# Performance work log

Measured on AMD Instinct MI355X. Metric: run time of the kernel, lower is better.

## Reference

```python
import jax, jax.numpy as jnp
import numpy as np

N, H, W = 8, 64, 64
CIN = 512    # latent_size_prev == conv_insize
COUT = 512   # latent_size == conv_outsize
Z = 512      # latent vector dim


def setup_inputs() -> dict:
    key = jax.random.key(0)
    ks = jax.random.split(key, 6)
    data = jax.random.normal(ks[0], (N, H, W, CIN), dtype=jnp.float32)
    latent = jax.random.normal(ks[1], (N, Z), dtype=jnp.float32)
    dense_w = jax.random.normal(ks[2], (Z, CIN), dtype=jnp.float32)
    dense_b = jnp.ones((CIN,), dtype=jnp.float32)  # ones_initializer per StyleBlock2
    conv_w = jax.random.normal(ks[3], (3, 3, CIN, COUT), dtype=jnp.float32)
    bias = jnp.zeros((1, 1, 1, COUT), dtype=jnp.float32)
    noise_coef = jnp.zeros((1, 1, 1, COUT), dtype=jnp.float32)
    noise = jax.random.normal(ks[4], (N, H, W, COUT), dtype=jnp.float32)
    return {"data": data, "latent": latent, "dense_w": dense_w, "dense_b": dense_b,
            "conv_w": conv_w, "bias": bias, "noise_coef": noise_coef, "noise": noise}


def reference(data, latent, dense_w, dense_b, conv_w, bias, noise_coef, noise):
    # ScaledDense: style vector s = latent @ (W * sqrt(2/Z)) + b
    dense_coef = jnp.sqrt(2.0 / Z).astype(data.dtype)
    s = latent @ (dense_w * dense_coef) + dense_b           # [N, CIN]

    # modulate input by style
    x = data * s[:, None, None, :]                          # [N,H,W,CIN]

    conv_coef = jnp.sqrt(2.0 / (CIN * 9)).astype(data.dtype)
    w = conv_w * conv_coef                                  # [3,3,CIN,COUT]
    y = jax.lax.conv_general_dilated(
        x, w, window_strides=(1, 1), padding='SAME',
        dimension_numbers=('NHWC', 'HWIO', 'NHWC'))         # [N,H,W,COUT]

    # demodulation: sum_{k,k,cin} (w * s)^2 == (s^2) @ sum_{k,k} w^2
    w2 = jnp.sum(w * w, axis=(0, 1))                        # [CIN, COUT]
    d = jax.lax.rsqrt((s * s) @ w2 + 1e-8)                  # [N, COUT]
    y = y * d[:, None, None, :]

    y = y + bias + noise * noise_coef
    return jnp.where(y >= 0, y, 0.2 * y)  # leaky relu, alpha=0.2
```

## Files before the change

### kernel.cpp

```cpp
#include <hip/hip_runtime.h>
#include <stdint.h>

typedef unsigned short ushort_t;
typedef unsigned int uint_t;
typedef __bf16 bf16x8 __attribute__((ext_vector_type(8)));
typedef float f32x4 __attribute__((ext_vector_type(4)));

#define C2F 0.02083333333333333f

__device__ __forceinline__ float bf2f(unsigned short u) {
  union { unsigned int i; float f; } v; v.i = ((unsigned int)u) << 16; return v.f;
}
__device__ __forceinline__ unsigned short f2bf(float f) {
  union { float f; unsigned int i; } v; v.f = f;
  unsigned int r = v.i + 0x7FFFu + ((v.i >> 16) & 1u);
  return (unsigned short)(r >> 16);
}
__device__ __forceinline__ bool bf_mode(const void* dense_b) {
  return *(const uint_t*)dense_b == 0x3F803F80u;
}
__device__ __forceinline__ void async16(const void* g, void* l) {
  __builtin_amdgcn_global_load_lds(
      (const __attribute__((address_space(1))) unsigned int*)g,
      (__attribute__((address_space(3))) unsigned int*)l, 16, 0, 0);
}

__global__ void k_style_p(const void* __restrict__ latent, const void* __restrict__ dw,
                          const void* __restrict__ db, float* __restrict__ sp) {
  const bool bf = bf_mode(db);
  int c = blockIdx.x * 256 + threadIdx.x;
  int n = blockIdx.y, zc = blockIdx.z;
  int z0 = zc * 64;
  float acc = 0.f;
  if (bf) {
    const ushort_t* L = (const ushort_t*)latent;
    const ushort_t* W = (const ushort_t*)dw;
    for (int z = z0; z < z0 + 64; ++z) acc += bf2f(L[n * 512 + z]) * bf2f(W[z * 512 + c]);
  } else {
    const float* L = (const float*)latent;
    const float* W = (const float*)dw;
    for (int z = z0; z < z0 + 64; ++z) acc += L[n * 512 + z] * W[z * 512 + c];
  }
  sp[(zc * 8 + n) * 512 + c] = acc;
}

__global__ void k_style_f(const float* __restrict__ sp, const void* __restrict__ db,
                          float* __restrict__ s) {
  const bool bf = bf_mode(db);
  int c = blockIdx.x * 256 + threadIdx.x;
  int n = blockIdx.y;
  float acc = 0.f;
#pragma unroll
  for (int zc = 0; zc < 8; ++zc) acc += sp[(zc * 8 + n) * 512 + c];
  float bv = bf ? bf2f(((const ushort_t*)db)[c]) : ((const float*)db)[c];
  s[n * 512 + c] = acc * 0.0625f + bv;
}

__global__ void k_w2(const void* __restrict__ cw, const void* __restrict__ db,
                     float* __restrict__ w2) {
  const bool bf = bf_mode(db);
  int i = blockIdx.x * blockDim.x + threadIdx.x;
  float a = 0.f;
  if (bf) {
    const ushort_t* W = (const ushort_t*)cw;
    for (int t = 0; t < 9; ++t) { float v = bf2f(W[t * 262144 + i]); a += v * v; }
  } else {
    const float* W = (const float*)cw;
    for (int t = 0; t < 9; ++t) { float v = W[t * 262144 + i]; a += v * v; }
  }
  w2[i] = a;
}

__global__ void k_demod_p(const float* __restrict__ s, const float* __restrict__ w2,
                          float* __restrict__ qp) {
  int c = blockIdx.x * 256 + threadIdx.x;
  int n = blockIdx.y, kc = blockIdx.z;
  int k0 = kc * 64;
  float q = 0.f;
  for (int k = k0; k < k0 + 64; ++k) {
    float sv = s[n * 512 + k];
    q += sv * sv * w2[k * 512 + c];
  }
  qp[(kc * 8 + n) * 512 + c] = q;
}

__global__ void k_demod_f(const float* __restrict__ qp, float* __restrict__ dfac) {
  int c = blockIdx.x * 256 + threadIdx.x;
  int n = blockIdx.y;
  float q = 0.f;
#pragma unroll
  for (int kc = 0; kc < 8; ++kc) q += qp[(kc * 8 + n) * 512 + c];
  dfac[n * 512 + c] = C2F * rsqrtf(C2F * C2F * q + 1e-8f);
}

__global__ void k_wt(const void* __restrict__ cw, const void* __restrict__ db,
                     ushort_t* __restrict__ wT) {
  __shared__ ushort_t tile[64][66];
  const bool bf = bf_mode(db);
  int tap = blockIdx.z;
  int ci0 = blockIdx.y * 64, co0 = blockIdx.x * 64;
  int col = threadIdx.x & 63, r0 = threadIdx.x >> 6;
  if (bf) {
    const ushort_t* src = (const ushort_t*)cw + tap * 262144;
    for (int r = r0; r < 64; r += 4) tile[r][col] = src[(ci0 + r) * 512 + co0 + col];
  } else {
    const float* src = (const float*)cw + tap * 262144;
    for (int r = r0; r < 64; r += 4) tile[r][col] = f2bf(src[(ci0 + r) * 512 + co0 + col]);
  }
  __syncthreads();
  ushort_t* dst = wT + tap * 262144;
  for (int r = r0; r < 64; r += 4)
    dst[(co0 + r) * 512 + ci0 + col] = tile[col][r];
}

__global__ void k_xpad(const void* __restrict__ data, const void* __restrict__ db,
                       const float* __restrict__ s, ushort_t* __restrict__ xpad) {
  const bool bf = bf_mode(db);
  int idx = blockIdx.x * 256 + threadIdx.x;
  int c = (idx & 63) * 8;
  int p = idx >> 6;
  int wp = p % 66; int q = p / 66; int hp = q % 66; int n = q / 66;
  uint_t ov[4] = {0u, 0u, 0u, 0u};
  if ((unsigned)(hp - 1) < 64u && (unsigned)(wp - 1) < 64u) {
    const float4 s0 = *(const float4*)(s + n * 512 + c);
    const float4 s1 = *(const float4*)(s + n * 512 + c + 4);
    size_t src = (size_t)((n * 64 + (hp - 1)) * 64 + (wp - 1)) * 512 + c;
    float x[8];
    if (bf) {
      uint4 dv = *(const uint4*)((const ushort_t*)data + src);
      x[0] = bf2f((unsigned short)(dv.x & 0xFFFFu)); x[1] = bf2f((unsigned short)(dv.x >> 16));
      x[2] = bf2f((unsigned short)(dv.y & 0xFFFFu)); x[3] = bf2f((unsigned short)(dv.y >> 16));
      x[4] = bf2f((unsigned short)(dv.z & 0xFFFFu)); x[5] = bf2f((unsigned short)(dv.z >> 16));
      x[6] = bf2f((unsigned short)(dv.w & 0xFFFFu)); x[7] = bf2f((unsigned short)(dv.w >> 16));
    } else {
      const float* df = (const float*)data + src;
      float4 a = *(const float4*)df; float4 b = *(const float4*)(df + 4);
      x[0] = a.x; x[1] = a.y; x[2] = a.z; x[3] = a.w;
      x[4] = b.x; x[5] = b.y; x[6] = b.z; x[7] = b.w;
    }
    float sv[8] = {s0.x, s0.y, s0.z, s0.w, s1.x, s1.y, s1.z, s1.w};
#pragma unroll
    for (int j = 0; j < 4; ++j)
      ov[j] = (uint_t)f2bf(x[j * 2] * sv[j * 2]) |
              ((uint_t)f2bf(x[j * 2 + 1] * sv[j * 2 + 1]) << 16);
  }
  uint4 o; o.x = ov[0]; o.y = ov[1]; o.z = ov[2]; o.w = ov[3];
  *(uint4*)(xpad + (size_t)p * 512 + c) = o;
}

template <bool BF>
__device__ __forceinline__ void epi(
    const f32x4 (&acc)[2][4][2][2], const float* __restrict__ dfac,
    const void* __restrict__ bias, const void* __restrict__ ncoef,
    const void* __restrict__ noise, void* __restrict__ out,
    int n_img, int posBase, int coutBase, int lane, int wr, int wc) {
  const int rq = (lane >> 4) * 4;
#pragma unroll
  for (int nh = 0; nh < 2; ++nh)
#pragma unroll
  for (int fn = 0; fn < 2; ++fn) {
    const int cout = coutBase + wc * 64 + nh * 32 + fn * 16 + (lane & 15);
    const float dv = dfac[n_img * 512 + cout];
    const float bv = BF ? bf2f(((const ushort_t*)bias)[cout]) : ((const float*)bias)[cout];
    const float nc = BF ? bf2f(((const ushort_t*)ncoef)[cout]) : ((const float*)ncoef)[cout];
#pragma unroll
    for (int mh = 0; mh < 2; ++mh)
#pragma unroll
    for (int f = 0; f < 4; ++f) {
      const int m = wr * 128 + mh * 64 + f * 16 + rq;
#pragma unroll
      for (int r = 0; r < 4; ++r) {
        const size_t o = (size_t)(posBase + m + r) * 512 + cout;
        const float nv = BF ? bf2f(((const ushort_t*)noise)[o]) : ((const float*)noise)[o];
        float y = acc[mh][f][nh][fn][r] * dv + bv + nv * nc;
        y = (y >= 0.f) ? y : 0.2f * y;
        if (BF) ((ushort_t*)out)[o] = f2bf(y);
        else    ((float*)out)[o] = y;
      }
    }
  }
}

__global__ __launch_bounds__(512, 2) void k_conv(
    const ushort_t* __restrict__ xpad, const ushort_t* __restrict__ wT,
    const float* __restrict__ dfac, const void* __restrict__ bias,
    const void* __restrict__ ncoef, const void* __restrict__ noise,
    const void* __restrict__ db, void* __restrict__ out) {
  extern __shared__ ushort_t lds[];

  const int t = threadIdx.x;
  const int bid0 = blockIdx.x;
  const int bid = (bid0 & 7) * 32 + (bid0 >> 3);
  const int coutBase = (bid & 1) * 256;
  const int posBase = (bid >> 1) * 256;
  const int n_img = posBase >> 12;
  const int hh0 = (posBase >> 6) & 63;

  const int rt = t >> 3;
  const int c8 = ((t & 7) ^ (rt & 7)) * 8;
  const ushort_t* aPtr = xpad + ((size_t)((n_img * 66 + hh0) * 66 + rt) * 512 + c8);
  const int bRow = ((t >> 8) & 1) * 64 + ((t >> 3) & 31);
  const ushort_t* bPtr = wT + ((size_t)(coutBase + bRow) * 512 + c8);
  ushort_t* aLds = lds + t * 8;
  ushort_t* bLds = lds + 32768 + t * 8;

#define STG_A(slot, mh, kt) do { \
    const int tap_ = (kt) >> 3, kh_ = tap_ / 3, kw_ = tap_ - kh_ * 3, k0_ = ((kt) & 7) << 6; \
    async16(aPtr + ((((mh) + kh_) * 66 + kw_) * 512 + k0_), \
            aLds + (slot) * 16384 + (mh) * 4096); \
    async16(aPtr + ((((mh) + 2 + kh_) * 66 + kw_) * 512 + k0_), \
            aLds + (slot) * 16384 + ((mh) + 2) * 4096); \
  } while (0)
#define STG_B(slot, nh, kt) do { \
    const int tap_ = (kt) >> 3, k0_ = ((kt) & 7) << 6; \
    async16(bPtr + (tap_ * 262144 + (nh) * 16384 + k0_), \
            bLds + (slot) * 16384 + (nh) * 8192); \
    async16(bPtr + (tap_ * 262144 + (nh) * 16384 + 65536 + k0_), \
            bLds + (slot) * 16384 + (nh) * 8192 + 4096); \
  } while (0)

  STG_A(0, 0, 0); STG_B(0, 0, 0); STG_B(0, 1, 0); STG_A(0, 1, 0);
  STG_A(1, 0, 1); STG_B(1, 0, 1); STG_B(1, 1, 1);

  const int lane = t & 63, wid = t >> 6, wr = wid >> 2, wc = wid & 3;
  const int g16 = (lane >> 4) * 16, lrow = lane & 15, xv = (lane & 7) << 4;
  const char* LB = (const char*)lds;
  const int sbA0 = (((wr * 128 + lrow) * 128) + g16) ^ xv;
  const int sbA1 = (((wr * 128 + lrow) * 128) + 64 + g16) ^ xv;
  const int sbB0 = ((65536 + (wc * 32 + lrow) * 128) + g16) ^ xv;
  const int sbB1 = ((65536 + (wc * 32 + lrow) * 128) + 64 + g16) ^ xv;

  bf16x8 rA[4][2], rB0[2][2], rB1[2][2];
  f32x4 acc[2][4][2][2] = {};

#define LDA(mh, sB) do { _Pragma("unroll") for (int f = 0; f < 4; ++f) { \
    rA[f][0] = *(const bf16x8*)(LB + ((sB) + (mh) * 8192 + f * 2048 + sbA0)); \
    rA[f][1] = *(const bf16x8*)(LB + ((sB) + (mh) * 8192 + f * 2048 + sbA1)); } } while (0)
#define LDB(R, nh, sB) do { _Pragma("unroll") for (int fn = 0; fn < 2; ++fn) { \
    R[fn][0] = *(const bf16x8*)(LB + ((sB) + (nh) * 16384 + fn * 2048 + sbB0)); \
    R[fn][1] = *(const bf16x8*)(LB + ((sB) + (nh) * 16384 + fn * 2048 + sbB1)); } } while (0)
#define MM(mh, nh, RB) do { __builtin_amdgcn_s_setprio(1); \
    _Pragma("unroll") for (int f = 0; f < 4; ++f) \
    _Pragma("unroll") for (int fn = 0; fn < 2; ++fn) \
    _Pragma("unroll") for (int ks = 0; ks < 2; ++ks) \
      acc[mh][f][nh][fn] = __builtin_amdgcn_mfma_f32_16x16x32_bf16( \
          rA[f][ks], (RB)[fn][ks], acc[mh][f][nh][fn], 0, 0, 0); \
    __builtin_amdgcn_s_setprio(0); } while (0)
#define BAR()   __builtin_amdgcn_s_barrier()
#define LGKM0() do { asm volatile("s_waitcnt lgkmcnt(0)" ::: "memory"); \
    __builtin_amdgcn_sched_barrier(0); } while (0)
#define WAITV4() asm volatile("s_waitcnt vmcnt(4)" ::: "memory")
#define WAITV6() asm volatile("s_waitcnt vmcnt(6)" ::: "memory")

  WAITV6();
  BAR();
  LDA(0, 0); LDB(rB0, 0, 0);

#pragma unroll 1
  for (int it = 0; it < 36; ++it) {
    const int kt0 = 2 * it;
    const int ktA = kt0 + 1;
    const int ktB = (kt0 + 2 <= 71) ? kt0 + 2 : 71;
    const int ktC = (kt0 + 3 <= 71) ? kt0 + 3 : 71;
    LGKM0(); MM(0, 0, rB0);
    LDB(rB1, 1, 0);
    STG_A(1, 1, ktA); BAR();
    LGKM0(); MM(0, 1, rB1);
    LDA(1, 0);
    STG_A(0, 0, ktB); BAR();
    LGKM0(); MM(1, 1, rB1);
    STG_B(0, 0, ktB); BAR();
    MM(1, 0, rB0);
    WAITV4();
    LDA(0, 32768); LDB(rB0, 0, 32768);
    STG_B(0, 1, ktB); BAR();
    LGKM0(); MM(0, 0, rB0);
    LDB(rB1, 1, 32768);
    STG_A(0, 1, ktB); BAR();
    LGKM0(); MM(0, 1, rB1);
    LDA(1, 32768);
    STG_A(1, 0, ktC); BAR();
    LGKM0(); MM(1, 1, rB1);
    STG_B(1, 0, ktC); BAR();
    MM(1, 0, rB0);
    WAITV4();
    LDA(0, 0); LDB(rB0, 0, 0);
    STG_B(1, 1, ktC); BAR();
  }
  asm volatile("s_waitcnt vmcnt(0)" ::: "memory");

  if (bf_mode(db))
    epi<true>(acc, dfac, bias, ncoef, noise, out, n_img, posBase, coutBase, lane, wr, wc);
  else
    epi<false>(acc, dfac, bias, ncoef, noise, out, n_img, posBase, coutBase, lane, wr, wc);
#undef STG_A
#undef STG_B
#undef LDA
#undef LDB
#undef MM
#undef BAR
#undef LGKM0
#undef WAITV4
#undef WAITV6
}

extern "C" void kernel_launch(void* const* d_in, const int* in_sizes, int n_in,
                              void* d_out, int out_size, void* d_ws, size_t ws_size,
                              hipStream_t stream) {
  (void)in_sizes; (void)n_in; (void)out_size; (void)ws_size;
  const void* data    = d_in[0];
  const void* latent  = d_in[1];
  const void* dense_w = d_in[2];
  const void* dense_b = d_in[3];
  const void* conv_w  = d_in[4];
  const void* bias    = d_in[5];
  const void* ncoef   = d_in[6];
  const void* noise   = d_in[7];

  static int once = [] {
    (void)hipFuncSetAttribute((const void*)k_conv,
                              hipFuncAttributeMaxDynamicSharedMemorySize, 131072);
    return 0;
  }();
  (void)once;

  float* s    = (float*)d_ws;
  float* dfac = s + 4096;
  float* w2   = dfac + 4096;
  float* sp   = w2 + 262144;
  float* qp   = sp + 32768;
  ushort_t* wT   = (ushort_t*)(qp + 32768);
  ushort_t* xpad = wT + 2359296;

  k_style_p<<<dim3(2, 8, 8), 256, 0, stream>>>(latent, dense_w, dense_b, sp);
  k_style_f<<<dim3(2, 8), 256, 0, stream>>>(sp, dense_b, s);
  k_w2<<<1024, 256, 0, stream>>>(conv_w, dense_b, w2);
  k_wt<<<dim3(8, 8, 9), 256, 0, stream>>>(conv_w, dense_b, wT);
  k_demod_p<<<dim3(2, 8, 8), 256, 0, stream>>>(s, w2, qp);
  k_demod_f<<<dim3(2, 8), 256, 0, stream>>>(qp, dfac);
  k_xpad<<<8712, 256, 0, stream>>>(data, dense_b, s, xpad);
  k_conv<<<256, 512, 131072, stream>>>(xpad, wT, dfac, bias, ncoef, noise, dense_b, d_out);
}
```

Baseline: 389.7 us.

## Merge preprocessing kernels into one launch and reorder conv K loop

The style partial product, w^2 reduction and weight transpose now run in a single block-partitioned kernel, and the two-stage demodulation collapses into one kernel that loops over all 512 inputs. This cuts five launches down to two and drops the qp scratch buffer. The conv K-step order changes from tap-major to channel-chunk-major, so consecutive steps walk the nine taps within one 64-channel chunk, which may change cache locality. The single-stage demod kernel runs only 16 blocks with a long serial loop, which could be slower than the split version.

```diff
diff --git a/kernel.cpp b/kernel.cpp
--- a/kernel.cpp
+++ b/kernel.cpp
@@ -25,23 +25,58 @@
       (__attribute__((address_space(3))) unsigned int*)l, 16, 0, 0);
 }
 
-__global__ void k_style_p(const void* __restrict__ latent, const void* __restrict__ dw,
-                          const void* __restrict__ db, float* __restrict__ sp) {
+__global__ void k_pre(const void* __restrict__ latent, const void* __restrict__ dw,
+                      const void* __restrict__ cw, const void* __restrict__ db,
+                      float* __restrict__ sp, float* __restrict__ w2,
+                      ushort_t* __restrict__ wT) {
+  __shared__ ushort_t tile[64][66];
   const bool bf = bf_mode(db);
-  int c = blockIdx.x * 256 + threadIdx.x;
-  int n = blockIdx.y, zc = blockIdx.z;
-  int z0 = zc * 64;
-  float acc = 0.f;
-  if (bf) {
-    const ushort_t* L = (const ushort_t*)latent;
-    const ushort_t* W = (const ushort_t*)dw;
-    for (int z = z0; z < z0 + 64; ++z) acc += bf2f(L[n * 512 + z]) * bf2f(W[z * 512 + c]);
+  const int b = blockIdx.x;
+  const int t = threadIdx.x;
+  if (b < 128) {
+    int cb = b & 1, n = (b >> 1) & 7, zc = b >> 4;
+    int c = cb * 256 + t;
+    int z0 = zc * 64;
+    float acc = 0.f;
+    if (bf) {
+      const ushort_t* L = (const ushort_t*)latent;
+      const ushort_t* W = (const ushort_t*)dw;
+      for (int z = z0; z < z0 + 64; ++z) acc += bf2f(L[n * 512 + z]) * bf2f(W[z * 512 + c]);
+    } else {
+      const float* L = (const float*)latent;
+      const float* W = (const float*)dw;
+      for (int z = z0; z < z0 + 64; ++z) acc += L[n * 512 + z] * W[z * 512 + c];
+    }
+    sp[(zc * 8 + n) * 512 + c] = acc;
+  } else if (b < 1152) {
+    int i = (b - 128) * 256 + t;
+    float a = 0.f;
+    if (bf) {
+      const ushort_t* W = (const ushort_t*)cw;
+      for (int tp = 0; tp < 9; ++tp) { float v = bf2f(W[tp * 262144 + i]); a += v * v; }
+    } else {
+      const float* W = (const float*)cw;
+      for (int tp = 0; tp < 9; ++tp) { float v = W[tp * 262144 + i]; a += v * v; }
+    }
+    w2[i] = a;
   } else {
-    const float* L = (const float*)latent;
-    const float* W = (const float*)dw;
-    for (int z = z0; z < z0 + 64; ++z) acc += L[n * 512 + z] * W[z * 512 + c];
-  }
-  sp[(zc * 8 + n) * 512 + c] = acc;
+    int b2 = b - 1152;
+    int tap = b2 >> 6;
+    int rem = b2 & 63;
+    int ci0 = ((rem >> 3) & 7) * 64, co0 = (rem & 7) * 64;
+    int col = t & 63, r0 = t >> 6;
+    if (bf) {
+      const ushort_t* src = (const ushort_t*)cw + tap * 262144;
+      for (int r = r0; r < 64; r += 4) tile[r][col] = src[(ci0 + r) * 512 + co0 + col];
+    } else {
+      const float* src = (const float*)cw + tap * 262144;
+      for (int r = r0; r < 64; r += 4) tile[r][col] = f2bf(src[(ci0 + r) * 512 + co0 + col]);
+    }
+    __syncthreads();
+    ushort_t* dst = wT + tap * 262144;
+    for (int r = r0; r < 64; r += 4)
+      dst[(co0 + r) * 512 + ci0 + col] = tile[col][r];
+  }
 }
 
 __global__ void k_style_f(const float* __restrict__ sp, const void* __restrict__ db,
@@ -56,61 +91,16 @@
   s[n * 512 + c] = acc * 0.0625f + bv;
 }
 
-__global__ void k_w2(const void* __restrict__ cw, const void* __restrict__ db,
-                     float* __restrict__ w2) {
-  const bool bf = bf_mode(db);
-  int i = blockIdx.x * blockDim.x + threadIdx.x;
-  float a = 0.f;
-  if (bf) {
-    const ushort_t* W = (const ushort_t*)cw;
-    for (int t = 0; t < 9; ++t) { float v = bf2f(W[t * 262144 + i]); a += v * v; }
-  } else {
-    const float* W = (const float*)cw;
-    for (int t = 0; t < 9; ++t) { float v = W[t * 262144 + i]; a += v * v; }
-  }
-  w2[i] = a;
-}
-
-__global__ void k_demod_p(const float* __restrict__ s, const float* __restrict__ w2,
-                          float* __restrict__ qp) {
-  int c = blockIdx.x * 256 + threadIdx.x;
-  int n = blockIdx.y, kc = blockIdx.z;
-  int k0 = kc * 64;
-  float q = 0.f;
-  for (int k = k0; k < k0 + 64; ++k) {
-    float sv = s[n * 512 + k];
-    q += sv * sv * w2[k * 512 + c];
-  }
-  qp[(kc * 8 + n) * 512 + c] = q;
-}
-
-__global__ void k_demod_f(const float* __restrict__ qp, float* __restrict__ dfac) {
+__global__ void k_demod(const float* __restrict__ s, const float* __restrict__ w2,
+                        float* __restrict__ dfac) {
   int c = blockIdx.x * 256 + threadIdx.x;
   int n = blockIdx.y;
   float q = 0.f;
-#pragma unroll
-  for (int kc = 0; kc < 8; ++kc) q += qp[(kc * 8 + n) * 512 + c];
+  for (int k = 0; k < 512; ++k) {
+    float sv = s[n * 512 + k];
+    q += sv * sv * w2[k * 512 + c];
+  }
   dfac[n * 512 + c] = C2F * rsqrtf(C2F * C2F * q + 1e-8f);
-}
-
-__global__ void k_wt(const void* __restrict__ cw, const void* __restrict__ db,
-                     ushort_t* __restrict__ wT) {
-  __shared__ ushort_t tile[64][66];
-  const bool bf = bf_mode(db);
-  int tap = blockIdx.z;
-  int ci0 = blockIdx.y * 64, co0 = blockIdx.x * 64;
-  int col = threadIdx.x & 63, r0 = threadIdx.x >> 6;
-  if (bf) {
-    const ushort_t* src = (const ushort_t*)cw + tap * 262144;
-    for (int r = r0; r < 64; r += 4) tile[r][col] = src[(ci0 + r) * 512 + co0 + col];
-  } else {
-    const float* src = (const float*)cw + tap * 262144;
-    for (int r = r0; r < 64; r += 4) tile[r][col] = f2bf(src[(ci0 + r) * 512 + co0 + col]);
-  }
-  __syncthreads();
-  ushort_t* dst = wT + tap * 262144;
-  for (int r = r0; r < 64; r += 4)
-    dst[(co0 + r) * 512 + ci0 + col] = tile[col][r];
 }
 
 __global__ void k_xpad(const void* __restrict__ data, const void* __restrict__ db,
@@ -205,14 +195,15 @@
   ushort_t* bLds = lds + 32768 + t * 8;
 
 #define STG_A(slot, mh, kt) do { \
-    const int tap_ = (kt) >> 3, kh_ = tap_ / 3, kw_ = tap_ - kh_ * 3, k0_ = ((kt) & 7) << 6; \
+    const int cc_ = (kt) / 9, tap_ = (kt) - cc_ * 9; \
+    const int kh_ = tap_ / 3, kw_ = tap_ - kh_ * 3, k0_ = cc_ << 6; \
     async16(aPtr + ((((mh) + kh_) * 66 + kw_) * 512 + k0_), \
             aLds + (slot) * 16384 + (mh) * 4096); \
     async16(aPtr + ((((mh) + 2 + kh_) * 66 + kw_) * 512 + k0_), \
             aLds + (slot) * 16384 + ((mh) + 2) * 4096); \
   } while (0)
 #define STG_B(slot, nh, kt) do { \
-    const int tap_ = (kt) >> 3, k0_ = ((kt) & 7) << 6; \
+    const int cc_ = (kt) / 9, tap_ = (kt) - cc_ * 9, k0_ = cc_ << 6; \
     async16(bPtr + (tap_ * 262144 + (nh) * 16384 + k0_), \
             bLds + (slot) * 16384 + (nh) * 8192); \
     async16(bPtr + (tap_ * 262144 + (nh) * 16384 + 65536 + k0_), \
@@ -328,16 +319,12 @@
   float* dfac = s + 4096;
   float* w2   = dfac + 4096;
   float* sp   = w2 + 262144;
-  float* qp   = sp + 32768;
-  ushort_t* wT   = (ushort_t*)(qp + 32768);
+  ushort_t* wT   = (ushort_t*)(sp + 32768);
   ushort_t* xpad = wT + 2359296;
 
-  k_style_p<<<dim3(2, 8, 8), 256, 0, stream>>>(latent, dense_w, dense_b, sp);
+  k_pre<<<1728, 256, 0, stream>>>(latent, dense_w, conv_w, dense_b, sp, w2, wT);
   k_style_f<<<dim3(2, 8), 256, 0, stream>>>(sp, dense_b, s);
-  k_w2<<<1024, 256, 0, stream>>>(conv_w, dense_b, w2);
-  k_wt<<<dim3(8, 8, 9), 256, 0, stream>>>(conv_w, dense_b, wT);
-  k_demod_p<<<dim3(2, 8, 8), 256, 0, stream>>>(s, w2, qp);
-  k_demod_f<<<dim3(2, 8), 256, 0, stream>>>(qp, dfac);
+  k_demod<<<dim3(2, 8), 256, 0, stream>>>(s, w2, dfac);
   k_xpad<<<8712, 256, 0, stream>>>(data, dense_b, s, xpad);
   k_conv<<<256, 512, 131072, stream>>>(xpad, wT, dfac, bias, ncoef, noise, dense_b, d_out);
 }
```

Measured after the change: 396.9 us. No clear change (+1.8%).

## Switch conv GEMM to 32x32x16 MFMA with reorganized LDS layout

Applied to the files above, without the earlier changes.

Replaces the 16x16x32 bf16 MFMA tiles with 32x32x16 MFMA, which changes the accumulator layout, the LDS fragment addressing (the XOR swizzle is dropped for a linear k-major layout) and the epilogue row mapping. The K loop order changes from tap-major to channel-chunk-major, and the global-to-LDS staging is rewritten to match. The aim is fewer MFMA issues and LDS reads per unit of work. Without the swizzle, LDS bank conflicts are a risk.

```diff
diff --git a/kernel.cpp b/kernel.cpp
--- a/kernel.cpp
+++ b/kernel.cpp
@@ -4,7 +4,7 @@
 typedef unsigned short ushort_t;
 typedef unsigned int uint_t;
 typedef __bf16 bf16x8 __attribute__((ext_vector_type(8)));
-typedef float f32x4 __attribute__((ext_vector_type(4)));
+typedef float f32x16 __attribute__((ext_vector_type(16)));
 
 #define C2F 0.02083333333333333f
 
@@ -150,29 +150,26 @@
 
 template <bool BF>
 __device__ __forceinline__ void epi(
-    const f32x4 (&acc)[2][4][2][2], const float* __restrict__ dfac,
+    const f32x16 (&acc)[4][2], const float* __restrict__ dfac,
     const void* __restrict__ bias, const void* __restrict__ ncoef,
     const void* __restrict__ noise, void* __restrict__ out,
     int n_img, int posBase, int coutBase, int lane, int wr, int wc) {
-  const int rq = (lane >> 4) * 4;
-#pragma unroll
-  for (int nh = 0; nh < 2; ++nh)
+  const int l31 = lane & 31, lh = (lane >> 5) * 4;
 #pragma unroll
   for (int fn = 0; fn < 2; ++fn) {
-    const int cout = coutBase + wc * 64 + nh * 32 + fn * 16 + (lane & 15);
+    const int cout = coutBase + wc * 64 + fn * 32 + l31;
     const float dv = dfac[n_img * 512 + cout];
     const float bv = BF ? bf2f(((const ushort_t*)bias)[cout]) : ((const float*)bias)[cout];
     const float nc = BF ? bf2f(((const ushort_t*)ncoef)[cout]) : ((const float*)ncoef)[cout];
 #pragma unroll
-    for (int mh = 0; mh < 2; ++mh)
-#pragma unroll
     for (int f = 0; f < 4; ++f) {
-      const int m = wr * 128 + mh * 64 + f * 16 + rq;
-#pragma unroll
-      for (int r = 0; r < 4; ++r) {
-        const size_t o = (size_t)(posBase + m + r) * 512 + cout;
+      const int posb = posBase + wr * 128 + f * 32 + lh;
+#pragma unroll
+      for (int r = 0; r < 16; ++r) {
+        const int row = (r & 3) + 8 * (r >> 2);
+        const size_t o = (size_t)(posb + row) * 512 + cout;
         const float nv = BF ? bf2f(((const ushort_t*)noise)[o]) : ((const float*)noise)[o];
-        float y = acc[mh][f][nh][fn][r] * dv + bv + nv * nc;
+        float y = acc[f][fn][r] * dv + bv + nv * nc;
         y = (y >= 0.f) ? y : 0.2f * y;
         if (BF) ((ushort_t*)out)[o] = f2bf(y);
         else    ((float*)out)[o] = y;
@@ -196,55 +193,48 @@
   const int n_img = posBase >> 12;
   const int hh0 = (posBase >> 6) & 63;
 
-  const int rt = t >> 3;
-  const int c8 = ((t & 7) ^ (rt & 7)) * 8;
-  const ushort_t* aPtr = xpad + ((size_t)((n_img * 66 + hh0) * 66 + rt) * 512 + c8);
-  const int bRow = ((t >> 8) & 1) * 64 + ((t >> 3) & 31);
-  const ushort_t* bPtr = wT + ((size_t)(coutBase + bRow) * 512 + c8);
+  const ushort_t* aP = xpad + ((size_t)((n_img * 66 + hh0) * 66 + (t & 63)) * 512 + (t >> 6) * 8);
+  const ushort_t* bP = wT + ((size_t)(coutBase + (t & 63)) * 512 + (t >> 6) * 8);
   ushort_t* aLds = lds + t * 8;
   ushort_t* bLds = lds + 32768 + t * 8;
 
 #define STG_A(slot, mh, kt) do { \
-    const int tap_ = (kt) >> 3, kh_ = tap_ / 3, kw_ = tap_ - kh_ * 3, k0_ = ((kt) & 7) << 6; \
-    async16(aPtr + ((((mh) + kh_) * 66 + kw_) * 512 + k0_), \
-            aLds + (slot) * 16384 + (mh) * 4096); \
-    async16(aPtr + ((((mh) + 2 + kh_) * 66 + kw_) * 512 + k0_), \
-            aLds + (slot) * 16384 + ((mh) + 2) * 4096); \
+    const int cc_ = (kt) / 9, tap_ = (kt) - cc_ * 9; \
+    const int kh_ = tap_ / 3, kw_ = tap_ - kh_ * 3; \
+    const int ko_ = (kh_ * 66 + kw_) * 512 + cc_ * 64; \
+    async16(aP + (ko_ + (mh) * 33792), aLds + (slot) * 16384 + (mh) * 4096); \
+    async16(aP + (ko_ + ((mh) + 2) * 33792), aLds + (slot) * 16384 + ((mh) + 2) * 4096); \
   } while (0)
-#define STG_B(slot, nh, kt) do { \
-    const int tap_ = (kt) >> 3, k0_ = ((kt) & 7) << 6; \
-    async16(bPtr + (tap_ * 262144 + (nh) * 16384 + k0_), \
-            bLds + (slot) * 16384 + (nh) * 8192); \
-    async16(bPtr + (tap_ * 262144 + (nh) * 16384 + 65536 + k0_), \
-            bLds + (slot) * 16384 + (nh) * 8192 + 4096); \
+#define STG_B(slot, bh, kt) do { \
+    const int cc_ = (kt) / 9, tap_ = (kt) - cc_ * 9; \
+    const int ko_ = tap_ * 262144 + cc_ * 64; \
+    async16(bP + (ko_ + (bh) * 32768), bLds + (slot) * 16384 + (bh) * 4096); \
+    async16(bP + (ko_ + ((bh) + 2) * 32768), bLds + (slot) * 16384 + ((bh) + 2) * 4096); \
   } while (0)
 
   STG_A(0, 0, 0); STG_B(0, 0, 0); STG_B(0, 1, 0); STG_A(0, 1, 0);
   STG_A(1, 0, 1); STG_B(1, 0, 1); STG_B(1, 1, 1);
 
   const int lane = t & 63, wid = t >> 6, wr = wid >> 2, wc = wid & 3;
-  const int g16 = (lane >> 4) * 16, lrow = lane & 15, xv = (lane & 7) << 4;
   const char* LB = (const char*)lds;
-  const int sbA0 = (((wr * 128 + lrow) * 128) + g16) ^ xv;
-  const int sbA1 = (((wr * 128 + lrow) * 128) + 64 + g16) ^ xv;
-  const int sbB0 = ((65536 + (wc * 32 + lrow) * 128) + g16) ^ xv;
-  const int sbB1 = ((65536 + (wc * 32 + lrow) * 128) + 64 + g16) ^ xv;
-
-  bf16x8 rA[4][2], rB0[2][2], rB1[2][2];
-  f32x4 acc[2][4][2][2] = {};
-
-#define LDA(mh, sB) do { _Pragma("unroll") for (int f = 0; f < 4; ++f) { \
-    rA[f][0] = *(const bf16x8*)(LB + ((sB) + (mh) * 8192 + f * 2048 + sbA0)); \
-    rA[f][1] = *(const bf16x8*)(LB + ((sB) + (mh) * 8192 + f * 2048 + sbA1)); } } while (0)
-#define LDB(R, nh, sB) do { _Pragma("unroll") for (int fn = 0; fn < 2; ++fn) { \
-    R[fn][0] = *(const bf16x8*)(LB + ((sB) + (nh) * 16384 + fn * 2048 + sbB0)); \
-    R[fn][1] = *(const bf16x8*)(LB + ((sB) + (nh) * 16384 + fn * 2048 + sbB1)); } } while (0)
-#define MM(mh, nh, RB) do { __builtin_amdgcn_s_setprio(1); \
-    _Pragma("unroll") for (int f = 0; f < 4; ++f) \
-    _Pragma("unroll") for (int fn = 0; fn < 2; ++fn) \
-    _Pragma("unroll") for (int ks = 0; ks < 2; ++ks) \
-      acc[mh][f][nh][fn] = __builtin_amdgcn_mfma_f32_16x16x32_bf16( \
-          rA[f][ks], (RB)[fn][ks], acc[mh][f][nh][fn], 0, 0, 0); \
+  const int sbA = 2 * wr * 8192 + (lane >> 5) * 1024 + (lane & 31) * 16;
+  const int sbB = 65536 + wc * 8192 + (lane >> 5) * 1024 + (lane & 31) * 16;
+
+  bf16x8 rA[2][4], rB0[4], rB1[4];
+  f32x16 acc[4][2] = {};
+
+#define LDA(p, sB) do { _Pragma("unroll") for (int fi = 0; fi < 2; ++fi) \
+    _Pragma("unroll") for (int ks = 0; ks < 4; ++ks) \
+      rA[fi][ks] = *(const bf16x8*)(LB + ((sB) + sbA + (p) * 8192 + fi * 512 + ks * 2048)); \
+  } while (0)
+#define LDB(R, fn, sB) do { _Pragma("unroll") for (int ks = 0; ks < 4; ++ks) \
+      R[ks] = *(const bf16x8*)(LB + ((sB) + sbB + (fn) * 512 + ks * 2048)); \
+  } while (0)
+#define MM(p, fn, RB) do { __builtin_amdgcn_s_setprio(1); \
+    _Pragma("unroll") for (int ks = 0; ks < 4; ++ks) \
+    _Pragma("unroll") for (int fi = 0; fi < 2; ++fi) \
+      acc[2 * (p) + fi][fn] = __builtin_amdgcn_mfma_f32_32x32x16_bf16( \
+          rA[fi][ks], (RB)[ks], acc[2 * (p) + fi][fn], 0, 0, 0); \
     __builtin_amdgcn_s_setprio(0); } while (0)
 #define BAR()   __builtin_amdgcn_s_barrier()
 #define LGKM0() do { asm volatile("s_waitcnt lgkmcnt(0)" ::: "memory"); \
```

Result: slower. 459.9 us (+18.0%).
